# Kernel tuning notes

Measured on AMD Instinct MI355X. Metric: run time of the kernel, lower is better.

The kernel has to match this reference:

```python
import jax, jax.numpy as jnp
import numpy as np

B, N, P, Q, E = 8, 5000, 256, 256, 160000


def _linear_params(k, out_d, in_d):
    # matches nn.init.normal_(std=0.1) weights, zero bias
    return 0.1 * jax.random.normal(k, (out_d, in_d), jnp.float32), jnp.zeros((out_d,), jnp.float32)


def setup_inputs() -> dict:
    key = jax.random.key(0)
    ks = jax.random.split(key, 8)
    u = jax.random.normal(ks[0], (B, N, P + Q), jnp.float32)
    src = jax.random.randint(ks[1], (E,), 0, N, dtype=jnp.int32)
    dst = jax.random.randint(ks[2], (E,), 0, N, dtype=jnp.int32)
    t = jnp.zeros((1,), jnp.float32)
    W_Fc, b_Fc = _linear_params(ks[3], P, P + Q)
    W_Fh, b_Fh = _linear_params(ks[4], Q, P + Q)
    W_Gc, b_Gc = _linear_params(ks[5], P, P + Q)
    W_Z, b_Z = _linear_params(ks[6], P, P + Q)
    W_A, b_A = _linear_params(ks[7], Q, 2 * Q)
    return dict(u=u, src=src, dst=dst, t=t,
                W_Fc=W_Fc, b_Fc=b_Fc, W_Fh=W_Fh, b_Fh=b_Fh,
                W_Gc=W_Gc, b_Gc=b_Gc, W_Z=W_Z, b_Z=b_Z,
                W_A=W_A, b_A=b_A)


def _neighbor_mean(h, src, dst):
    # h: [B, N, Q] -> mean over in-neighbors per node (zeros if no neighbors)
    hT = jnp.transpose(h, (1, 0, 2))            # [N, B, Q]
    msgs = hT[src]                              # [E, B, Q] gather
    summed = jax.ops.segment_sum(msgs, dst, num_segments=N)          # [N, B, Q]
    deg = jax.ops.segment_sum(jnp.ones((E,), h.dtype), dst, num_segments=N)  # [N]
    mean = summed / jnp.maximum(deg, 1.0)[:, None, None]
    return jnp.transpose(mean, (1, 0, 2))       # [B, N, Q]


def reference(u, src, dst, t, W_Fc, b_Fc, W_Fh, b_Fh, W_Gc, b_Gc, W_Z, b_Z, W_A, b_A):
    sp = jax.nn.softplus
    lin = lambda x, W, b: jnp.einsum('bnd,od->bno', x, W) + b
    c = u[:, :, :P]
    h = u[:, :, P:]
    agg = _neighbor_mean(h, src, dst)                           # [B, N, Q]
    h_ = sp(lin(jnp.concatenate([h, agg], axis=2), W_A, b_A))   # [B, N, Q]
    u_ = jnp.concatenate([c, h_], axis=2)                       # [B, N, P+Q]
    Fc = sp(lin(u_, W_Fc, b_Fc))
    Gc = sp(lin(u_, W_Gc, b_Gc))
    Zt = jnp.tanh(lin(u_, W_Z, b_Z))
    Fh = sp(lin(u_, W_Fh, b_Fh))
    dc = -Fc * c + Gc * Zt
    dh = -Fh * h
    # tangent projection: remove component of dc along c
    proj = jnp.sum(dc * c, axis=2, keepdims=True) / jnp.sum(c * c, axis=2, keepdims=True)
    dc = dc - proj * c
    return jnp.concatenate([dc, dh], axis=2)
```

## Files before the change

kernel.cpp:

```cpp
#include <hip/hip_runtime.h>
#include <math.h>

#define B_ 8
#define N_ 5000
#define E_ 160000
#define M_ 40000
#define K_ 512
#define XT_ 313

typedef __bf16 v8bf __attribute__((ext_vector_type(8)));
typedef float  v4f  __attribute__((ext_vector_type(4)));
typedef unsigned short u16x4v __attribute__((ext_vector_type(4)));
typedef unsigned short u16x8v __attribute__((ext_vector_type(8)));

__device__ __forceinline__ unsigned short f2b(float f){
  unsigned int u = __builtin_bit_cast(unsigned int, f);
  u += 0x7FFFu + ((u >> 16) & 1u);
  return (unsigned short)(u >> 16);
}
__device__ __forceinline__ float b2f(unsigned short s){
  return __builtin_bit_cast(float, ((unsigned int)s) << 16);
}
__device__ __forceinline__ float softplus_(float x){
  return (x > 15.0f) ? x : __logf(1.0f + __expf(x));
}
__device__ __forceinline__ float tanh_(float x){
  float e = __expf(2.0f*x);
  return 1.0f - 2.0f/(e + 1.0f);
}


__global__ __launch_bounds__(256) void zero_int2(int* a, int* b, int n){
  int i = blockIdx.x*256 + threadIdx.x;
  if (i < n){ a[i] = 0; b[i] = 0; }
}

__global__ __launch_bounds__(256) void convert_weights(
    const float* __restrict__ wA, const float* __restrict__ wFc,
    const float* __restrict__ wGc, const float* __restrict__ wZ,
    const float* __restrict__ wFh,
    const float* __restrict__ bFc, const float* __restrict__ bGc,
    const float* __restrict__ bZ,  const float* __restrict__ bFh,
    unsigned short* __restrict__ WA, unsigned short* __restrict__ Wall,
    float* __restrict__ biasP)
{
  int idx = blockIdx.x*256 + threadIdx.x;
  if (idx >= 655360){
    int j = idx - 655360;
    int mat = j >> 8, jj = j & 255;
    const float* bp = (mat == 0) ? bFc : (mat == 1) ? bGc : (mat == 2) ? bZ : bFh;
    biasP[j] = bp[jj];
    return;
  }
  int m = idx >> 17;
  int i = idx & 131071;
  float v;
  if      (m == 0) v = wA[i];
  else if (m == 1) v = wFc[i];
  else if (m == 2) v = wGc[i];
  else if (m == 3) v = wZ[i];
  else             v = wFh[i];
  unsigned short o = f2b(v);

  int n   = (m == 0) ? (i >> 9) : ((m - 1)*256 + (i >> 9));
  int col = i & 511;
  int y  = n >> 7, nn = n & 127;
  int cb = nn >> 4, lr = nn & 15;
  int kb = col >> 6, c6 = col & 63;
  int ch = c6 >> 3, e = c6 & 7;
  int ks = ch >> 2, lq = ch & 3;
  int lane = lq*16 + lr;
  size_t pidx = ((((size_t)(y*8 + kb)*2 + ks)*8 + cb)*64 + lane)*8 + e;
  if (m == 0) WA[pidx] = o;
  else        Wall[pidx] = o;
}

__global__ __launch_bounds__(256) void convert_u(
    const float* __restrict__ u, unsigned short* __restrict__ cB,
    unsigned short* __restrict__ hT)
{
  int r = blockIdx.x*4 + (threadIdx.x >> 6);
  int l = threadIdx.x & 63;
  int n = r >> 3, b = r & 7;
  const float* up = u + (size_t)(b*N_ + n)*512 + l*4;
  float4 cf = *(const float4*)up;
  float4 hf = *(const float4*)(up + 256);
  u16x4v c4, h4;
  c4.x = f2b(cf.x); c4.y = f2b(cf.y); c4.z = f2b(cf.z); c4.w = f2b(cf.w);
  h4.x = f2b(hf.x); h4.y = f2b(hf.y); h4.z = f2b(hf.z); h4.w = f2b(hf.w);
  *(u16x4v*)(cB + (size_t)r*256 + l*4) = c4;
  *(u16x4v*)(hT + (size_t)r*256 + l*4) = h4;
}


__global__ __launch_bounds__(256) void hist_kernel(const int* __restrict__ dst, int* __restrict__ deg){
  int e = blockIdx.x*256 + threadIdx.x;
  atomicAdd(&deg[dst[e]], 1);
}

__global__ __launch_bounds__(256) void scan_kernel(
    const int* __restrict__ deg, int* __restrict__ row_start, float* __restrict__ inv_deg)
{
  __shared__ int sums[256];
  int t = threadIdx.x;
  int base = t*20;
  int cnt[20];
  int local = 0;
#pragma unroll
  for (int i = 0; i < 20; ++i){
    int n = base + i;
    int d = (n < N_) ? deg[n] : 0;
    cnt[i] = d; local += d;
  }
  sums[t] = local; __syncthreads();
  for (int s = 1; s < 256; s <<= 1){
    int v = (t >= s) ? sums[t - s] : 0;
    __syncthreads();
    sums[t] += v;
    __syncthreads();
  }
  int prefix = (t == 0) ? 0 : sums[t-1];
#pragma unroll
  for (int i = 0; i < 20; ++i){
    int n = base + i;
    if (n < N_){
      row_start[n] = prefix;
      int d = cnt[i];
      inv_deg[n] = 1.0f / (float)((d > 1) ? d : 1);
      prefix += d;
    }
  }
  if (t == 255) row_start[N_] = prefix;
}

__global__ __launch_bounds__(256) void fill_kernel(
    const int* __restrict__ src, const int* __restrict__ dst,
    const int* __restrict__ row_start, int* __restrict__ cursor, int* __restrict__ csr)
{
  int e = blockIdx.x*256 + threadIdx.x;
  int d = dst[e];
  int p = atomicAdd(&cursor[d], 1);
  csr[row_start[d] + p] = src[e];
}

__global__ __launch_bounds__(256) void gather_bn_kernel(
    const unsigned short* __restrict__ hT, const int* __restrict__ csr,
    const int* __restrict__ row_start, const float* __restrict__ inv_deg,
    unsigned short* __restrict__ aggT)
{
  const int id = blockIdx.x;
  const int bb = id & 7;
  const int g  = id >> 3;
  const int tid = threadIdx.x;
  const int n = g*4 + (tid >> 6);
  const int l = tid & 63;
  const int half = l >> 5, li = l & 31;
  const size_t coff = (size_t)bb*256 + li*8;
  const int e0 = row_start[n], e1 = row_start[n+1];

  float acc[8] = {};
  int e = e0;
  for (; e + 3 < e1; e += 4){
    const int s0 = csr[e + half];
    const int s1 = csr[e + 2 + half];
    u16x8v v0 = *(const u16x8v*)(hT + (size_t)s0*2048 + coff);
    u16x8v v1 = *(const u16x8v*)(hT + (size_t)s1*2048 + coff);
#pragma unroll
    for (int i = 0; i < 8; ++i) acc[i] += b2f(v0[i]) + b2f(v1[i]);
  }
  for (; e < e1; e += 2){
    const int idx = e + half;
    u16x8v v = {};
    if (idx < e1){
      const int s = csr[idx];
      v = *(const u16x8v*)(hT + (size_t)s*2048 + coff);
    }
#pragma unroll
    for (int i = 0; i < 8; ++i) acc[i] += b2f(v[i]);
  }
#pragma unroll
  for (int i = 0; i < 8; ++i) acc[i] += __shfl_xor(acc[i], 32, 64);

  if (half == 0){
    const float inv = inv_deg[n];
    u16x8v o;
#pragma unroll
    for (int i = 0; i < 8; ++i) o[i] = f2b(acc[i]*inv);
    *(u16x8v*)(aggT + (size_t)n*2048 + coff) = o;
  }
}


__device__ __forceinline__ void stage_a(
    const unsigned short* __restrict__ As, int m0, int ak,
    int srow, int schunk, int w, unsigned short* lbuf)
{
#pragma unroll
  for (int i = 0; i < 4; ++i){
    const unsigned short* gp = As + (size_t)(m0 + i*32 + srow)*256 + ak + schunk*8;
    unsigned short* lp = lbuf + (i*32 + w*8)*64;
    __builtin_amdgcn_global_load_lds((const __attribute__((address_space(1))) void*)gp,
                                     (__attribute__((address_space(3))) void*)lp, 16, 0, 0);
  }
}

__device__ __forceinline__ void load_b(
    const unsigned short* __restrict__ Bp, int y, int kb, int wc, int l, v8bf (&b)[8])
{
#pragma unroll
  for (int ks = 0; ks < 2; ++ks)
#pragma unroll
    for (int ct = 0; ct < 4; ++ct)
      b[ks*4+ct] = *(const v8bf*)(Bp +
          ((((size_t)(y*8 + kb)*2 + ks)*8 + wc*4 + ct)*64 + l)*8);
}

__device__ __forceinline__ void compute_tile(
    const unsigned short* lA, int wr, int lq, int lr,
    const v8bf (&bb)[8], v4f (&acc)[4][4])
{
#pragma unroll
  for (int ks = 0; ks < 2; ++ks){
    v8bf a[4];
#pragma unroll
    for (int rt = 0; rt < 4; ++rt){
      const int ar = wr*64 + rt*16 + lr;
      a[rt] = *(const v8bf*)(lA + ar*64 + (((ks*4 + lq) ^ (ar & 7)))*8);
    }
#pragma unroll
    for (int rt = 0; rt < 4; ++rt)
#pragma unroll
      for (int ct = 0; ct < 4; ++ct)
        acc[rt][ct] = __builtin_amdgcn_mfma_f32_16x16x32_bf16(a[rt], bb[ks*4+ct], acc[rt][ct], 0, 0, 0);
  }
}

template<int MODE>
__global__ __launch_bounds__(256, 3) void gemm_tiled(
    const unsigned short* __restrict__ A0, const unsigned short* __restrict__ A1,
    const unsigned short* __restrict__ Bp, const float* __restrict__ bias,
    unsigned short* dstp)
{
  const int id = blockIdx.x;
  int x, y;
  if (MODE == 1){
    const int u6 = id & 63;
    y = u6 >> 3;
    x = (id >> 6)*8 + (u6 & 7);
  } else {
    const int u4 = id & 15;
    y = u4 >> 3;
    x = (id >> 4)*8 + (u4 & 7);
  }
  if (x >= XT_) return;

  __shared__ unsigned short lds[24576];

  const int tid = threadIdx.x;
  const int w  = tid >> 6, l = tid & 63;
  const int wr = w >> 1,  wc = w & 1;
  const int lq = l >> 4,  lr = l & 15;
  const int m0 = x * 128;
  const int n0 = y * 128;

  const int srow   = tid >> 3;
  const int schunk = (tid & 7) ^ (srow & 7);

  v4f acc[4][4] = {};
  v8bf b0[8], b1[8];

  stage_a(A0, m0, 0, srow, schunk, w, lds);
  asm volatile("" ::: "memory");
  load_b(Bp, y, 0, wc, l, b0);
  asm volatile("" ::: "memory");
  stage_a(A0, m0, 64, srow, schunk, w, lds + 8192);
  asm volatile("s_waitcnt vmcnt(12)" ::: "memory");
  __builtin_amdgcn_s_barrier();
  __builtin_amdgcn_sched_barrier(0);

#pragma unroll
  for (int kb = 0; kb < 7; ++kb){
    const int kp = kb + 2;
    if (kp < 8)
      stage_a((kp < 4) ? A0 : A1, m0, (kp & 3)*64, srow, schunk, w,
              lds + (kp % 3)*8192);
    asm volatile("" ::: "memory");
    if ((kb + 1) & 1) load_b(Bp, y, kb + 1, wc, l, b1);
    else              load_b(Bp, y, kb + 1, wc, l, b0);
    if (kb & 1) compute_tile(lds + (kb % 3)*8192, wr, lq, lr, b1, acc);
    else        compute_tile(lds + (kb % 3)*8192, wr, lq, lr, b0, acc);
    asm volatile("s_waitcnt vmcnt(12)" ::: "memory");
    __builtin_amdgcn_s_barrier();
    __builtin_amdgcn_sched_barrier(0);
  }
  compute_tile(lds + (7 % 3)*8192, wr, lq, lr, b1, acc);

  float bv[4];
#pragma unroll
  for (int ct = 0; ct < 4; ++ct) bv[ct] = bias[n0 + wc*64 + ct*16 + lr];

  const bool is_tanh = (MODE == 1) && ((y >> 1) == 2);

  __syncthreads();
#pragma unroll
  for (int rt = 0; rt < 4; ++rt){
#pragma unroll
    for (int ct = 0; ct < 4; ++ct){
      const int col = wc*64 + ct*16 + lr;
#pragma unroll
      for (int reg = 0; reg < 4; ++reg){
        const int row = wr*64 + rt*16 + lq*4 + reg;
        const float xv = acc[rt][ct][reg] + bv[ct];
        const float v = is_tanh ? tanh_(xv) : softplus_(xv);
        lds[row*136 + col] = f2b(v);
      }
    }
  }
  __syncthreads();

#pragma unroll
  for (int i = 0; i < 8; ++i){
    const int row = i*16 + (tid >> 4);
    const int r = m0 + row;
    if (r < M_){
      const uint4 v = *(const uint4*)(lds + row*136 + (tid & 15)*8);
      if (MODE == 0){
        *(uint4*)(dstp + (size_t)r*256 + n0 + (tid & 15)*8) = v;
      } else {
        const int n = r >> 3, b = r & 7;
        *(uint4*)(dstp + ((size_t)b*N_ + n)*1024 + n0 + (tid & 15)*8) = v;
      }
    }
  }
}


__global__ __launch_bounds__(256) void epilogue_kernel(
    const unsigned short* act, const float* __restrict__ u, float* out)
{
  int r = blockIdx.x*4 + (threadIdx.x >> 6);
  int l = threadIdx.x & 63;
  int n = r >> 3, b = r & 7;
  const size_t rr = (size_t)(b*N_ + n);
  const unsigned short* arow = act + rr*1024;
  const float* urow = u + rr*512;
  float* orow = out + rr*512;

  u16x4v fc4 = *(const u16x4v*)(arow +        l*4);
  u16x4v gc4 = *(const u16x4v*)(arow + 256 +  l*4);
  u16x4v z4  = *(const u16x4v*)(arow + 512 +  l*4);
  u16x4v fh4 = *(const u16x4v*)(arow + 768 +  l*4);
  float4 c4f = *(const float4*)(urow + l*4);
  float4 h4f = *(const float4*)(urow + 256 + l*4);

  float c[4] = {c4f.x, c4f.y, c4f.z, c4f.w};
  float h[4] = {h4f.x, h4f.y, h4f.z, h4f.w};
  float dc[4], fh[4];
  float num = 0.f, den = 0.f;
#pragma unroll
  for (int i = 0; i < 4; ++i){
    float fc = b2f(fc4[i]), gc = b2f(gc4[i]), z = b2f(z4[i]);
    fh[i] = b2f(fh4[i]);
    dc[i] = -fc*c[i] + gc*z;
    num += dc[i]*c[i];
    den += c[i]*c[i];
  }
#pragma unroll
  for (int s = 1; s < 64; s <<= 1){
    num += __shfl_xor(num, s, 64);
    den += __shfl_xor(den, s, 64);
  }
  const float proj = num / den;

  float4 o, oh;
  o.x = dc[0] - proj*c[0]; o.y = dc[1] - proj*c[1];
  o.z = dc[2] - proj*c[2]; o.w = dc[3] - proj*c[3];
  oh.x = -fh[0]*h[0]; oh.y = -fh[1]*h[1];
  oh.z = -fh[2]*h[2]; oh.w = -fh[3]*h[3];
  *(float4*)(orow + l*4) = o;
  *(float4*)(orow + 256 + l*4) = oh;
}


extern "C" void kernel_launch(void* const* d_in, const int* in_sizes, int n_in,
                              void* d_out, int out_size, void* d_ws, size_t ws_size,
                              hipStream_t stream) {
  const float* u    = (const float*)d_in[0];
  const int*   src  = (const int*)d_in[1];
  const int*   dst  = (const int*)d_in[2];
  const float* wFc  = (const float*)d_in[4];
  const float* bFc  = (const float*)d_in[5];
  const float* wFh  = (const float*)d_in[6];
  const float* bFh  = (const float*)d_in[7];
  const float* wGc  = (const float*)d_in[8];
  const float* bGc  = (const float*)d_in[9];
  const float* wZ   = (const float*)d_in[10];
  const float* bZ   = (const float*)d_in[11];
  const float* wA   = (const float*)d_in[12];
  const float* bA   = (const float*)d_in[13];
  float* out = (float*)d_out;
  unsigned short* act = (unsigned short*)d_out;

  char* W = (char*)d_ws;
  unsigned short* hT   = (unsigned short*)(W + 0);
  unsigned short* cB   = (unsigned short*)(W + 20480000);
  unsigned short* aggT = (unsigned short*)(W + 40960000);
  unsigned short* hB   = (unsigned short*)(W + 61440000);
  unsigned short* WA   = (unsigned short*)(W + 81920000);
  unsigned short* Wall = (unsigned short*)(W + 82182144);
  float* biasP   = (float*)(W + 83230720);
  int* deg       = (int*)(W + 83234816);
  int* row_start = (int*)(W + 83255296);
  int* cursor    = (int*)(W + 83275776);
  int* csr       = (int*)(W + 83296256);
  float* inv_deg = (float*)(W + 83936256);

  zero_int2<<<(N_ + 255)/256, 256, 0, stream>>>(deg, cursor, N_);
  convert_weights<<<2564, 256, 0, stream>>>(wA, wFc, wGc, wZ, wFh,
                                            bFc, bGc, bZ, bFh, WA, Wall, biasP);
  convert_u<<<M_/4, 256, 0, stream>>>(u, cB, hT);
  hist_kernel<<<E_/256, 256, 0, stream>>>(dst, deg);
  scan_kernel<<<1, 256, 0, stream>>>(deg, row_start, inv_deg);
  fill_kernel<<<E_/256, 256, 0, stream>>>(src, dst, row_start, cursor, csr);

  gather_bn_kernel<<<8*1250, 256, 0, stream>>>(hT, csr, row_start, inv_deg, aggT);

  gemm_tiled<0><<<40*16, 256, 0, stream>>>(hT, aggT, WA, bA, hB);
  gemm_tiled<1><<<40*64, 256, 0, stream>>>(cB, hB, Wall, biasP, act);

  epilogue_kernel<<<M_/4, 256, 0, stream>>>(act, u, out);
}
```

Measured before the change: 352.7 us.

## Pre-swizzle c and h_ activations into MFMA fragment layout, load A directly

convert_u now stages rows through shared memory and writes c in the MFMA A-fragment tiled layout. The first GEMM also writes h_ in that layout. The big GEMM then reads A operands straight from global memory into registers, with no LDS staging, async global-to-LDS copies or barriers in its main loop. This removes LDS traffic and synchronisation from the dominant GEMM, at the cost of losing the software pipelining. Its global loads are no longer overlapped with MFMA work except through occupancy.

```diff
diff --git a/kernel.cpp b/kernel.cpp
--- a/kernel.cpp
+++ b/kernel.cpp
@@ -79,17 +79,40 @@
     const float* __restrict__ u, unsigned short* __restrict__ cB,
     unsigned short* __restrict__ hT)
 {
-  int r = blockIdx.x*4 + (threadIdx.x >> 6);
-  int l = threadIdx.x & 63;
-  int n = r >> 3, b = r & 7;
-  const float* up = u + (size_t)(b*N_ + n)*512 + l*4;
-  float4 cf = *(const float4*)up;
-  float4 hf = *(const float4*)(up + 256);
-  u16x4v c4, h4;
-  c4.x = f2b(cf.x); c4.y = f2b(cf.y); c4.z = f2b(cf.z); c4.w = f2b(cf.w);
-  h4.x = f2b(hf.x); h4.y = f2b(hf.y); h4.z = f2b(hf.z); h4.w = f2b(hf.w);
-  *(u16x4v*)(cB + (size_t)r*256 + l*4) = c4;
-  *(u16x4v*)(hT + (size_t)r*256 + l*4) = h4;
+  __shared__ unsigned short ls[16*520];
+  const int t = threadIdx.x;
+  const int r0 = blockIdx.x * 16;
+  const int rr = t >> 4, seg = t & 15;
+  {
+    const int r = r0 + rr;
+    const int n = r >> 3, b = r & 7;
+    const float* src = u + ((size_t)b*N_ + n)*512 + seg*32;
+    unsigned short* dst = ls + rr*520 + seg*32;
+#pragma unroll
+    for (int i = 0; i < 8; ++i){
+      float4 f = *(const float4*)(src + i*4);
+      u16x4v o4;
+      o4.x = f2b(f.x); o4.y = f2b(f.y); o4.z = f2b(f.z); o4.w = f2b(f.w);
+      *(u16x4v*)(dst + i*4) = o4;
+    }
+  }
+  __syncthreads();
+  {
+    const int r = r0 + rr;
+    const int q0 = seg*16;
+    u16x8v v0 = *(const u16x8v*)(ls + rr*520 + 256 + q0);
+    u16x8v v1 = *(const u16x8v*)(ls + rr*520 + 256 + q0 + 8);
+    *(u16x8v*)(hT + (size_t)r*256 + q0) = v0;
+    *(u16x8v*)(hT + (size_t)r*256 + q0 + 8) = v1;
+  }
+#pragma unroll
+  for (int it = 0; it < 2; ++it){
+    const int ch = t + it*256;
+    const int kc = ch >> 6, lane = ch & 63;
+    const int lr2 = lane & 15, lq2 = lane >> 4;
+    u16x8v v = *(const u16x8v*)(ls + lr2*520 + kc*32 + lq2*8);
+    *(u16x8v*)(cB + (((size_t)blockIdx.x*8 + kc)*64 + lane)*8) = v;
+  }
 }
 
 
@@ -191,6 +214,18 @@
 }
 
 
+__device__ __forceinline__ void load_b(
+    const unsigned short* __restrict__ Bp, int y, int kb, int wc, int l, v8bf (&b)[8])
+{
+#pragma unroll
+  for (int ks = 0; ks < 2; ++ks)
+#pragma unroll
+    for (int ct = 0; ct < 4; ++ct)
+      b[ks*4+ct] = *(const v8bf*)(Bp +
+          ((((size_t)(y*8 + kb)*2 + ks)*8 + wc*4 + ct)*64 + l)*8);
+}
+
+
 __device__ __forceinline__ void stage_a(
     const unsigned short* __restrict__ As, int m0, int ak,
     int srow, int schunk, int w, unsigned short* lbuf)
@@ -204,18 +239,7 @@
   }
 }
 
-__device__ __forceinline__ void load_b(
-    const unsigned short* __restrict__ Bp, int y, int kb, int wc, int l, v8bf (&b)[8])
-{
-#pragma unroll
-  for (int ks = 0; ks < 2; ++ks)
-#pragma unroll
-    for (int ct = 0; ct < 4; ++ct)
-      b[ks*4+ct] = *(const v8bf*)(Bp +
-          ((((size_t)(y*8 + kb)*2 + ks)*8 + wc*4 + ct)*64 + l)*8);
-}
-
-__device__ __forceinline__ void compute_tile(
+__device__ __forceinline__ void compute_tile_lds(
     const unsigned short* lA, int wr, int lq, int lr,
     const v8bf (&bb)[8], v4f (&acc)[4][4])
 {
@@ -235,23 +259,15 @@
   }
 }
 
-template<int MODE>
-__global__ __launch_bounds__(256, 3) void gemm_tiled(
+__global__ __launch_bounds__(256, 3) void gemm_small(
     const unsigned short* __restrict__ A0, const unsigned short* __restrict__ A1,
     const unsigned short* __restrict__ Bp, const float* __restrict__ bias,
     unsigned short* dstp)
 {
   const int id = blockIdx.x;
-  int x, y;
-  if (MODE == 1){
-    const int u6 = id & 63;
-    y = u6 >> 3;
-    x = (id >> 6)*8 + (u6 & 7);
-  } else {
-    const int u4 = id & 15;
-    y = u4 >> 3;
-    x = (id >> 4)*8 + (u4 & 7);
-  }
+  const int u4 = id & 15;
+  const int y = u4 >> 3;
+  const int x = (id >> 4)*8 + (u4 & 7);
   if (x >= XT_) return;
 
   __shared__ unsigned short lds[24576];
@@ -269,7 +285,7 @@
   v4f acc[4][4] = {};
   v8bf b0[8], b1[8];
 
-  stage_a(A0, m0, 0, srow, schunk, w, lds);
+  stage_a(A0, m0, 0,  srow, schunk, w, lds);
   asm volatile("" ::: "memory");
   load_b(Bp, y, 0, wc, l, b0);
   asm volatile("" ::: "memory");
@@ -287,19 +303,96 @@
     asm volatile("" ::: "memory");
     if ((kb + 1) & 1) load_b(Bp, y, kb + 1, wc, l, b1);
     else              load_b(Bp, y, kb + 1, wc, l, b0);
-    if (kb & 1) compute_tile(lds + (kb % 3)*8192, wr, lq, lr, b1, acc);
-    else        compute_tile(lds + (kb % 3)*8192, wr, lq, lr, b0, acc);
+    if (kb & 1) compute_tile_lds(lds + (kb % 3)*8192, wr, lq, lr, b1, acc);
+    else        compute_tile_lds(lds + (kb % 3)*8192, wr, lq, lr, b0, acc);
     asm volatile("s_waitcnt vmcnt(12)" ::: "memory");
     __builtin_amdgcn_s_barrier();
     __builtin_amdgcn_sched_barrier(0);
   }
-  compute_tile(lds + (7 % 3)*8192, wr, lq, lr, b1, acc);
+  compute_tile_lds(lds + 8192, wr, lq, lr, b1, acc);
 
   float bv[4];
 #pragma unroll
   for (int ct = 0; ct < 4; ++ct) bv[ct] = bias[n0 + wc*64 + ct*16 + lr];
 
-  const bool is_tanh = (MODE == 1) && ((y >> 1) == 2);
+  __syncthreads();
+#pragma unroll
+  for (int rt = 0; rt < 4; ++rt){
+#pragma unroll
+    for (int ct = 0; ct < 4; ++ct){
+      const int col = wc*64 + ct*16 + lr;
+#pragma unroll
+      for (int reg = 0; reg < 4; ++reg){
+        const int row = wr*64 + rt*16 + lq*4 + reg;
+        const float xv = acc[rt][ct][reg] + bv[ct];
+        lds[row*136 + col] = f2b(softplus_(xv));
+      }
+    }
+  }
+  __syncthreads();
+
+#pragma unroll
+  for (int i = 0; i < 8; ++i){
+    const int row = i*16 + (tid >> 4);
+    const int r = m0 + row;
+    if (r < M_){
+      const uint4 v = *(const uint4*)(lds + row*136 + (tid & 15)*8);
+      const int c0 = n0 + (tid & 15)*8;
+      const int kc = c0 >> 5;
+      const int lane = ((c0 >> 3) & 3)*16 + (tid >> 4);
+      *(uint4*)(dstp + (((size_t)(r >> 4)*8 + kc)*64 + lane)*8) = v;
+    }
+  }
+}
+
+__global__ __launch_bounds__(256, 3) void gemm_big(
+    const unsigned short* __restrict__ Ac, const unsigned short* __restrict__ Ah,
+    const unsigned short* __restrict__ Bp, const float* __restrict__ bias,
+    unsigned short* dstp)
+{
+  const int id = blockIdx.x;
+  const int u6 = id & 63;
+  const int y = u6 >> 3;
+  const int x = (id >> 6)*8 + (u6 & 7);
+  if (x >= XT_) return;
+
+  __shared__ unsigned short lds[17408];
+
+  const int tid = threadIdx.x;
+  const int w  = tid >> 6, l = tid & 63;
+  const int wr = w >> 1,  wc = w & 1;
+  const int lq = l >> 4,  lr = l & 15;
+  const int m0 = x * 128;
+  const int n0 = y * 128;
+
+  v4f acc[4][4] = {};
+
+#pragma unroll
+  for (int kb = 0; kb < 8; ++kb){
+    const unsigned short* Ap = (kb < 4) ? Ac : Ah;
+    v8bf b[8];
+    load_b(Bp, y, kb, wc, l, b);
+    v8bf a[2][4];
+#pragma unroll
+    for (int ks = 0; ks < 2; ++ks)
+#pragma unroll
+      for (int rt = 0; rt < 4; ++rt)
+        a[ks][rt] = *(const v8bf*)(Ap +
+            (((size_t)(x*8 + wr*4 + rt)*8 + (kb & 3)*2 + ks)*64 + l)*8);
+#pragma unroll
+    for (int ks = 0; ks < 2; ++ks)
+#pragma unroll
+      for (int rt = 0; rt < 4; ++rt)
+#pragma unroll
+        for (int ct = 0; ct < 4; ++ct)
+          acc[rt][ct] = __builtin_amdgcn_mfma_f32_16x16x32_bf16(a[ks][rt], b[ks*4+ct], acc[rt][ct], 0, 0, 0);
+  }
+
+  float bv[4];
+#pragma unroll
+  for (int ct = 0; ct < 4; ++ct) bv[ct] = bias[n0 + wc*64 + ct*16 + lr];
+
+  const bool is_tanh = ((y >> 1) == 2);
 
   __syncthreads();
 #pragma unroll
@@ -324,12 +417,8 @@
     const int r = m0 + row;
     if (r < M_){
       const uint4 v = *(const uint4*)(lds + row*136 + (tid & 15)*8);
-      if (MODE == 0){
-        *(uint4*)(dstp + (size_t)r*256 + n0 + (tid & 15)*8) = v;
-      } else {
-        const int n = r >> 3, b = r & 7;
-        *(uint4*)(dstp + ((size_t)b*N_ + n)*1024 + n0 + (tid & 15)*8) = v;
-      }
+      const int n = r >> 3, b2 = r & 7;
+      *(uint4*)(dstp + ((size_t)b2*N_ + n)*1024 + n0 + (tid & 15)*8) = v;
     }
   }
 }
@@ -418,15 +507,15 @@
   zero_int2<<<(N_ + 255)/256, 256, 0, stream>>>(deg, cursor, N_);
   convert_weights<<<2564, 256, 0, stream>>>(wA, wFc, wGc, wZ, wFh,
                                             bFc, bGc, bZ, bFh, WA, Wall, biasP);
-  convert_u<<<M_/4, 256, 0, stream>>>(u, cB, hT);
+  convert_u<<<M_/16, 256, 0, stream>>>(u, cB, hT);
   hist_kernel<<<E_/256, 256, 0, stream>>>(dst, deg);
   scan_kernel<<<1, 256, 0, stream>>>(deg, row_start, inv_deg);
   fill_kernel<<<E_/256, 256, 0, stream>>>(src, dst, row_start, cursor, csr);
 
   gather_bn_kernel<<<8*1250, 256, 0, stream>>>(hT, csr, row_start, inv_deg, aggT);
 
-  gemm_tiled<0><<<40*16, 256, 0, stream>>>(hT, aggT, WA, bA, hB);
-  gemm_tiled<1><<<40*64, 256, 0, stream>>>(cB, hB, Wall, biasP, act);
+  gemm_small<<<40*16, 256, 0, stream>>>(hT, aggT, WA, bA, hB);
+  gemm_big<<<40*64, 256, 0, stream>>>(cB, hB, Wall, biasP, act);
 
   epilogue_kernel<<<M_/4, 256, 0, stream>>>(act, u, out);
 }
```

Result: slower. 370.3 us (+5.0%).
